# Performance work log

Measured on AMD Instinct MI355X. Metric: run time of the kernel, lower is better.

Reference implementation:

```python
import jax, jax.numpy as jnp
import numpy as np
from jax import lax

B, P, C = 2, 512, 5                 # images, proposals/img, classes (incl. background)
IN_FEAT, REP = 12544, 1024          # 256*7*7 pooled features; TwoMLPHead width
H_IMG = W_IMG = 800.0
SCORE_THRESH, NMS_THRESH, DET_PER_IMG = 0.05, 0.5, 100
MIN_SIZE = 0.01
WX, WY, WW, WH = 10.0, 10.0, 5.0, 5.0
BBOX_CLIP = float(np.log(1000.0 / 16.0))
NEG = -1e9


def _make_boxes(key, n):
    k1, k2, k3, k4 = jax.random.split(key, 4)
    cx = jax.random.uniform(k1, (n,)) * W_IMG
    cy = jax.random.uniform(k2, (n,)) * H_IMG
    bw = jax.random.uniform(k3, (n,)) * 180.0 + 20.0
    bh = jax.random.uniform(k4, (n,)) * 180.0 + 20.0
    x1 = jnp.clip(cx - bw / 2, 0.0, W_IMG)
    y1 = jnp.clip(cy - bh / 2, 0.0, H_IMG)
    x2 = jnp.clip(cx + bw / 2, 0.0, W_IMG)
    y2 = jnp.clip(cy + bh / 2, 0.0, H_IMG)
    return jnp.stack([x1, y1, x2, y2], -1).astype(jnp.float32)


def setup_inputs() -> dict:
    ks = jax.random.split(jax.random.key(0), 12)
    box_features = jax.random.normal(ks[0], (B * P, IN_FEAT), jnp.float32)
    proposals = jnp.stack([_make_boxes(ks[1 + i], P) for i in range(B)])
    def w(k, shp):
        return (jax.random.normal(k, shp, jnp.float32) / np.sqrt(shp[0])).astype(jnp.float32)
    return {
        'box_features': box_features,
        'proposals': proposals,
        'W1': w(ks[3], (IN_FEAT, REP)), 'b1': jnp.zeros((REP,), jnp.float32),
        'W2': w(ks[4], (REP, REP)),     'b2': jnp.zeros((REP,), jnp.float32),
        'Wc': w(ks[5], (REP, C)),       'bc': jnp.zeros((C,), jnp.float32),
        'Wb': w(ks[6], (REP, 4 * C)),   'bb': jnp.zeros((4 * C,), jnp.float32),
    }


def box_iou(a, b):
    area_a = (a[:, 2] - a[:, 0]) * (a[:, 3] - a[:, 1])
    area_b = (b[:, 2] - b[:, 0]) * (b[:, 3] - b[:, 1])
    lt = jnp.maximum(a[:, None, :2], b[None, :, :2])
    rb = jnp.minimum(a[:, None, 2:], b[None, :, 2:])
    wh = jnp.clip(rb - lt, 0.0)
    inter = wh[..., 0] * wh[..., 1]
    return inter / (area_a[:, None] + area_b[None, :] - inter + 1e-9)


def decode(reg, props):
    # reg: [N, C, 4] raw deltas; props: [N, 4] xyxy  (torchvision BoxCoder.decode)
    w = props[:, 2] - props[:, 0]
    h = props[:, 3] - props[:, 1]
    cx = props[:, 0] + 0.5 * w
    cy = props[:, 1] + 0.5 * h
    dx, dy = reg[..., 0] / WX, reg[..., 1] / WY
    dw = jnp.minimum(reg[..., 2] / WW, BBOX_CLIP)
    dh = jnp.minimum(reg[..., 3] / WH, BBOX_CLIP)
    pcx = dx * w[:, None] + cx[:, None]
    pcy = dy * h[:, None] + cy[:, None]
    pw = jnp.exp(dw) * w[:, None]
    ph = jnp.exp(dh) * h[:, None]
    return jnp.stack([pcx - 0.5 * pw, pcy - 0.5 * ph, pcx + 0.5 * pw, pcy + 0.5 * ph], -1)


def postprocess_one(boxes, scores, labels):
    # boxes [M,4] (already clipped), scores [M], labels [M] int; fixed-size output.
    M = boxes.shape[0]
    ws = boxes[:, 2] - boxes[:, 0]
    hs = boxes[:, 3] - boxes[:, 1]
    valid = (scores > SCORE_THRESH) & (ws >= MIN_SIZE) & (hs >= MIN_SIZE)
    order = jnp.argsort(-scores)
    b, s, l, v = boxes[order], scores[order], labels[order], valid[order]
    # batched (per-class) NMS via class-offset trick
    off = l.astype(b.dtype)[:, None] * (max(H_IMG, W_IMG) + 1.0)
    iou = box_iou(b + off, b + off)
    idxs = jnp.arange(M)

    def body(i, keep):
        sup = (iou[i] > NMS_THRESH) & keep[i] & (idxs > i)
        return keep & ~sup

    keep = lax.fori_loop(0, M, body, v)
    sc = jnp.where(keep, s, NEG)
    top_s, top_i = lax.top_k(sc, DET_PER_IMG)
    ok = top_s > NEG / 2
    tb = jnp.where(ok[:, None], b[top_i], 0.0)
    tl = jnp.where(ok, l[top_i], 0)
    ts = jnp.where(ok, top_s, 0.0)
    return tb, ts, tl


def reference(box_features, proposals, W1, b1, W2, b2, Wc, bc, Wb, bb):
    # box_head: TwoMLPHead
    h = jax.nn.relu(box_features @ W1 + b1)
    h = jax.nn.relu(h @ W2 + b2)
    # box_predictor
    class_logits = h @ Wc + bc                       # [N, C]
    box_regression = (h @ Wb + bb).reshape(-1, C, 4)  # [N, C, 4]
    props = proposals.reshape(-1, 4)
    pred = decode(box_regression, props)             # [N, C, 4]
    # clip to image
    pred = jnp.stack([
        jnp.clip(pred[..., 0], 0.0, W_IMG), jnp.clip(pred[..., 1], 0.0, H_IMG),
        jnp.clip(pred[..., 2], 0.0, W_IMG), jnp.clip(pred[..., 3], 0.0, H_IMG)], -1)
    scores = jax.nn.softmax(class_logits, -1)        # [N, C]
    # drop background class, flatten proposal-major (matches torch reshape(-1,4))
    pb = pred[:, 1:, :].reshape(B, P * (C - 1), 4)
    sc = scores[:, 1:].reshape(B, P * (C - 1))
    labels = jnp.tile(jnp.arange(1, C, dtype=jnp.int32), P)  # [M]
    boxes_o, scores_o, labels_o = jax.vmap(postprocess_one, in_axes=(0, 0, None))(pb, sc, labels)
    return boxes_o, scores_o, labels_o
```

## Files before the change

kernel.cpp:

```cpp
#include <hip/hip_runtime.h>
#include <math.h>

#define NROWS 1024
#define K1    12544
#define REP   1024
#define NDET  2048
#define DETS  100
#define BBOX_CLIP_F 4.135166556742356f
#define LDA   40

typedef __attribute__((ext_vector_type(8))) short bf16x8;
typedef __attribute__((ext_vector_type(4))) float f32x4;

__device__ __forceinline__ unsigned short rne_bf16(float x) {
  unsigned u = __float_as_uint(x);
  u += 0x7fffu + ((u >> 16) & 1u);
  return (unsigned short)(u >> 16);
}
__device__ __forceinline__ float bf16f(unsigned short h) {
  return __uint_as_float(((unsigned)h) << 16);
}

__global__ __launch_bounds__(256) void transpose_bf16(
    const float* __restrict__ W, unsigned short* __restrict__ WTh,
    unsigned short* __restrict__ WTl, int K, int N) {
  __shared__ unsigned short th[32 * 36], tl[32 * 36];
  const int k0 = blockIdx.x * 32, n0 = blockIdx.y * 32;
  const int t = threadIdx.x;
  const int r = t >> 3, c4 = (t & 7) << 2;
  float4 v = *(const float4*)&W[(size_t)(k0 + r) * N + n0 + c4];
  float fv[4] = {v.x, v.y, v.z, v.w};
#pragma unroll
  for (int j = 0; j < 4; ++j) {
    unsigned short h = rne_bf16(fv[j]);
    th[(c4 + j) * 36 + r] = h;
    tl[(c4 + j) * 36 + r] = rne_bf16(fv[j] - bf16f(h));
  }
  __syncthreads();
  ushort4 oh = *(ushort4*)&th[r * 36 + c4];
  ushort4 ol = *(ushort4*)&tl[r * 36 + c4];
  *(ushort4*)&WTh[(size_t)(n0 + r) * K + k0 + c4] = oh;
  *(ushort4*)&WTl[(size_t)(n0 + r) * K + k0 + c4] = ol;
}

__global__ __launch_bounds__(256) void gemm_mfma(
    const float* __restrict__ A, const unsigned short* __restrict__ BTh,
    const unsigned short* __restrict__ BTl, float* __restrict__ T,
    int K, int stepsPerZ) {
  __shared__ unsigned short Ash[128 * LDA], Asl[128 * LDA];
  __shared__ unsigned short Bsh[128 * LDA], Bsl[128 * LDA];
  const int tid = threadIdx.x;
  const int bm = blockIdx.x * 128, bn = blockIdx.y * 128;
  const int k0 = blockIdx.z * stepsPerZ * 32;
  const int w = tid >> 6, l = tid & 63;
  const int wr = (w >> 1) * 64, wc = (w & 1) * 64;
  const int fr = l & 15, fk = (l >> 4) * 8;
  const int srow = tid >> 2, skq = tid & 3;
  f32x4 acc[4][4];
#pragma unroll
  for (int m = 0; m < 4; ++m)
#pragma unroll
    for (int n = 0; n < 4; ++n) acc[m][n] = (f32x4){0.f, 0.f, 0.f, 0.f};

  for (int s = 0; s < stepsPerZ; ++s) {
    const int kk = k0 + s * 32;
#pragma unroll
    for (int half = 0; half < 2; ++half) {
      const int row = srow + half * 64;
      const float* ap = A + (size_t)(bm + row) * K + kk + skq * 8;
      float4 f0 = *(const float4*)ap;
      float4 f1 = *(const float4*)(ap + 4);
      float fv[8] = {f0.x, f0.y, f0.z, f0.w, f1.x, f1.y, f1.z, f1.w};
      unsigned hp[4], lp[4];
#pragma unroll
      for (int j = 0; j < 4; ++j) {
        unsigned short h0 = rne_bf16(fv[2 * j]), h1 = rne_bf16(fv[2 * j + 1]);
        float l0 = fv[2 * j] - bf16f(h0), l1 = fv[2 * j + 1] - bf16f(h1);
        hp[j] = (unsigned)h0 | ((unsigned)h1 << 16);
        lp[j] = (unsigned)rne_bf16(l0) | ((unsigned)rne_bf16(l1) << 16);
      }
      *(uint4*)&Ash[row * LDA + skq * 8] = make_uint4(hp[0], hp[1], hp[2], hp[3]);
      *(uint4*)&Asl[row * LDA + skq * 8] = make_uint4(lp[0], lp[1], lp[2], lp[3]);
      *(uint4*)&Bsh[row * LDA + skq * 8] =
          *(const uint4*)&BTh[(size_t)(bn + row) * K + kk + skq * 8];
      *(uint4*)&Bsl[row * LDA + skq * 8] =
          *(const uint4*)&BTl[(size_t)(bn + row) * K + kk + skq * 8];
    }
    __syncthreads();
    bf16x8 ah[4], al[4], bh[4], bl[4];
#pragma unroll
    for (int m = 0; m < 4; ++m) {
      ah[m] = *(const bf16x8*)&Ash[(wr + m * 16 + fr) * LDA + fk];
      al[m] = *(const bf16x8*)&Asl[(wr + m * 16 + fr) * LDA + fk];
    }
#pragma unroll
    for (int n = 0; n < 4; ++n) {
      bh[n] = *(const bf16x8*)&Bsh[(wc + n * 16 + fr) * LDA + fk];
      bl[n] = *(const bf16x8*)&Bsl[(wc + n * 16 + fr) * LDA + fk];
    }
#pragma unroll
    for (int m = 0; m < 4; ++m)
#pragma unroll
      for (int n = 0; n < 4; ++n) {
        acc[m][n] = __builtin_amdgcn_mfma_f32_16x16x32_bf16(ah[m], bh[n], acc[m][n], 0, 0, 0);
        acc[m][n] = __builtin_amdgcn_mfma_f32_16x16x32_bf16(ah[m], bl[n], acc[m][n], 0, 0, 0);
        acc[m][n] = __builtin_amdgcn_mfma_f32_16x16x32_bf16(al[m], bh[n], acc[m][n], 0, 0, 0);
      }
    __syncthreads();
  }
  float* Tz = T + (size_t)blockIdx.z * (NROWS * REP);
#pragma unroll
  for (int m = 0; m < 4; ++m) {
    const int r0 = bm + wr + m * 16 + ((l >> 4) << 2);
#pragma unroll
    for (int n = 0; n < 4; ++n) {
      const int c = bn + wc + n * 16 + fr;
#pragma unroll
      for (int j = 0; j < 4; ++j) Tz[(size_t)(r0 + j) * REP + c] = acc[m][n][j];
    }
  }
}

__global__ __launch_bounds__(256) void combine8_relu(
    const float* __restrict__ T, const float* __restrict__ bias, float* __restrict__ H) {
  const int i = blockIdx.x * 256 + threadIdx.x;
  const int MN4 = NROWS * REP / 4;
  const float4* t = (const float4*)T;
  float4 s0 = t[i];
#pragma unroll
  for (int z = 1; z < 8; ++z) {
    float4 v = t[i + z * MN4];
    s0.x += v.x; s0.y += v.y; s0.z += v.z; s0.w += v.w;
  }
  float4 bs = ((const float4*)bias)[i & 255];
  float4 r;
  r.x = fmaxf(s0.x + bs.x, 0.f);
  r.y = fmaxf(s0.y + bs.y, 0.f);
  r.z = fmaxf(s0.z + bs.z, 0.f);
  r.w = fmaxf(s0.w + bs.w, 0.f);
  ((float4*)H)[i] = r;
}

__global__ __launch_bounds__(256) void gemm64(
    const float* __restrict__ A, const float* __restrict__ W,
    float* __restrict__ T, int K, int N, int kChunk) {
  __shared__ float As[32][68];
  __shared__ float Bs[32][64];
  const int tid = threadIdx.x;
  const int bm = blockIdx.x * 64, bn = blockIdx.y * 64;
  const int k0 = blockIdx.z * kChunk;
  const int tx = tid & 15, ty = tid >> 4;
  const int ar = tid >> 3;
  const int ac = (tid & 7) << 2;
  const int br = tid >> 4;
  const int bc = (tid & 15) << 2;
  float acc[4][4] = {{0.f,0.f,0.f,0.f},{0.f,0.f,0.f,0.f},{0.f,0.f,0.f,0.f},{0.f,0.f,0.f,0.f}};
  for (int kk = k0; kk < k0 + kChunk; kk += 32) {
    float4 a0 = *(const float4*)&A[(size_t)(bm + ar) * K + kk + ac];
    float4 a1 = *(const float4*)&A[(size_t)(bm + ar + 32) * K + kk + ac];
    float4 b0 = *(const float4*)&W[(size_t)(kk + br) * N + bn + bc];
    float4 b1 = *(const float4*)&W[(size_t)(kk + br + 16) * N + bn + bc];
    As[ac+0][ar] = a0.x; As[ac+1][ar] = a0.y; As[ac+2][ar] = a0.z; As[ac+3][ar] = a0.w;
    As[ac+0][ar+32] = a1.x; As[ac+1][ar+32] = a1.y; As[ac+2][ar+32] = a1.z; As[ac+3][ar+32] = a1.w;
    *(float4*)&Bs[br][bc]    = b0;
    *(float4*)&Bs[br+16][bc] = b1;
    __syncthreads();
#pragma unroll
    for (int k = 0; k < 32; ++k) {
      float4 av = *(const float4*)&As[k][ty << 2];
      float4 bv = *(const float4*)&Bs[k][tx << 2];
      float a_[4] = {av.x, av.y, av.z, av.w};
      float b_[4] = {bv.x, bv.y, bv.z, bv.w};
#pragma unroll
      for (int i = 0; i < 4; ++i)
#pragma unroll
        for (int j = 0; j < 4; ++j)
          acc[i][j] = fmaf(a_[i], b_[j], acc[i][j]);
    }
    __syncthreads();
  }
  float* Tz = T + (size_t)blockIdx.z * NROWS * REP;
#pragma unroll
  for (int i = 0; i < 4; ++i) {
    float4 v = make_float4(acc[i][0], acc[i][1], acc[i][2], acc[i][3]);
    *(float4*)&Tz[(size_t)(bm + (ty << 2) + i) * N + bn + (tx << 2)] = v;
  }
}

__global__ __launch_bounds__(256) void combine_relu(
    const float* __restrict__ T, const float* __restrict__ bias, float* __restrict__ H) {
  const int i = blockIdx.x * 256 + threadIdx.x;
  const int MN4 = NROWS * REP / 4;
  const float4* t = (const float4*)T;
  float4 a = t[i], b = t[i + MN4], c = t[i + 2 * MN4], d = t[i + 3 * MN4];
  float4 bs = ((const float4*)bias)[i & 255];
  float4 r;
  r.x = fmaxf(((a.x + b.x) + (c.x + d.x)) + bs.x, 0.f);
  r.y = fmaxf(((a.y + b.y) + (c.y + d.y)) + bs.y, 0.f);
  r.z = fmaxf(((a.z + b.z) + (c.z + d.z)) + bs.z, 0.f);
  r.w = fmaxf(((a.w + b.w) + (c.w + d.w)) + bs.w, 0.f);
  ((float4*)H)[i] = r;
}

__global__ __launch_bounds__(256) void heads_kernel(
    const float* __restrict__ H2, const float* __restrict__ Wc, const float* __restrict__ bcv,
    const float* __restrict__ Wb, const float* __restrict__ bbv,
    const float* __restrict__ props, float* __restrict__ pb, float* __restrict__ sc) {
  const int n = blockIdx.x;
  __shared__ float hrow[REP];
  __shared__ float part[25][8];
  __shared__ float outv[25];
  __shared__ float smax[5];
  const int tid = threadIdx.x;
  ((float4*)hrow)[tid] = ((const float4*)(H2 + (size_t)n * REP))[tid];
  __syncthreads();
  if (tid < 200) {
    const int o = tid >> 3, s = tid & 7;
    float a = 0.f;
    if (o < 5) {
      const float* w = Wc + o;
      for (int k = s * 128; k < s * 128 + 128; ++k) a = fmaf(hrow[k], w[(size_t)k * 5], a);
    } else {
      const float* w = Wb + (o - 5);
      for (int k = s * 128; k < s * 128 + 128; ++k) a = fmaf(hrow[k], w[(size_t)k * 20], a);
    }
    part[o][s] = a;
  }
  __syncthreads();
  if (tid < 25) {
    float a = ((part[tid][0] + part[tid][1]) + (part[tid][2] + part[tid][3]))
            + ((part[tid][4] + part[tid][5]) + (part[tid][6] + part[tid][7]));
    a += (tid < 5) ? bcv[tid] : bbv[tid - 5];
    outv[tid] = a;
  }
  __syncthreads();
  if (tid == 0) {
    float m = outv[0];
    for (int c = 1; c < 5; ++c) m = fmaxf(m, outv[c]);
    float e[5], ssum = 0.f;
    for (int c = 0; c < 5; ++c) { e[c] = expf(outv[c] - m); ssum += e[c]; }
    for (int c = 0; c < 5; ++c) smax[c] = e[c] / ssum;
  }
  __syncthreads();
  if (tid < 4) {
    const int c = tid + 1;
    const float* pr = props + (size_t)n * 4;
    const float x1 = pr[0], y1 = pr[1], x2 = pr[2], y2 = pr[3];
    const float w = x2 - x1, h = y2 - y1;
    const float cx = x1 + 0.5f * w, cy = y1 + 0.5f * h;
    const float r0 = outv[5 + c * 4 + 0], r1 = outv[5 + c * 4 + 1];
    const float r2 = outv[5 + c * 4 + 2], r3 = outv[5 + c * 4 + 3];
    const float dx = r0 / 10.0f, dy = r1 / 10.0f;
    const float dw = fminf(r2 / 5.0f, BBOX_CLIP_F);
    const float dh = fminf(r3 / 5.0f, BBOX_CLIP_F);
    const float pcx = dx * w + cx, pcy = dy * h + cy;
    const float pw = expf(dw) * w, ph = expf(dh) * h;
    float bx1 = pcx - 0.5f * pw, by1 = pcy - 0.5f * ph;
    float bx2 = pcx + 0.5f * pw, by2 = pcy + 0.5f * ph;
    bx1 = fminf(fmaxf(bx1, 0.f), 800.f);
    by1 = fminf(fmaxf(by1, 0.f), 800.f);
    bx2 = fminf(fmaxf(bx2, 0.f), 800.f);
    by2 = fminf(fmaxf(by2, 0.f), 800.f);
    const int img = n >> 9;
    const int pidx = ((n & 511) << 2) + (c - 1);
    float* o = pb + (size_t)(img * NDET + pidx) * 4;
    o[0] = bx1; o[1] = by1; o[2] = bx2; o[3] = by2;
    sc[img * NDET + pidx] = smax[c];
  }
}

__global__ __launch_bounds__(1024) void sort_kernel(
    const float* __restrict__ sc, unsigned* __restrict__ sidx) {
  const int b = blockIdx.x;
  __shared__ unsigned long long key[NDET];
  const int tid = threadIdx.x;
  for (int t = tid; t < NDET; t += 1024) {
    unsigned bits = __float_as_uint(sc[b * NDET + t]);
    key[t] = ((unsigned long long)bits << 32) | (unsigned)(~t);
  }
  __syncthreads();
  for (int k = 2; k <= NDET; k <<= 1) {
    for (int j = k >> 1; j > 0; j >>= 1) {
      for (int t = tid; t < NDET; t += 1024) {
        const int ixj = t ^ j;
        if (ixj > t) {
          const bool up = (t & k) == 0;
          unsigned long long a = key[t], bb_ = key[ixj];
          if ((a < bb_) == up) { key[t] = bb_; key[ixj] = a; }
        }
      }
      __syncthreads();
    }
  }
  for (int t = tid; t < NDET; t += 1024)
    sidx[b * NDET + t] = ~(unsigned)key[t];
}

__global__ __launch_bounds__(256) void prep_kernel(
    const unsigned* __restrict__ sidx, const float* __restrict__ pb, const float* __restrict__ sc,
    float* __restrict__ sbox, float* __restrict__ soff, float* __restrict__ sscore,
    float* __restrict__ sarea, float* __restrict__ slab, unsigned* __restrict__ vword) {
  const int b = blockIdx.y;
  const int i = blockIdx.x * 256 + threadIdx.x;
  const unsigned oi = sidx[b * NDET + i];
  const float* bx = pb + (size_t)(b * NDET + oi) * 4;
  const float x1 = bx[0], y1 = bx[1], x2 = bx[2], y2 = bx[3];
  const float s = sc[b * NDET + oi];
  const float lab = (float)((oi & 3) + 1);
  const bool valid = (s > 0.05f) && ((x2 - x1) >= 0.01f) && ((y2 - y1) >= 0.01f);
  const float off = lab * 801.0f;
  float* sb = sbox + (size_t)(b * NDET + i) * 4;
  sb[0] = x1; sb[1] = y1; sb[2] = x2; sb[3] = y2;
  float* so = soff + (size_t)(b * NDET + i) * 4;
  so[0] = x1 + off; so[1] = y1 + off; so[2] = x2 + off; so[3] = y2 + off;
  sscore[b * NDET + i] = s;
  sarea[b * NDET + i] = (x2 - x1) * (y2 - y1);
  slab[b * NDET + i] = lab;
  const unsigned long long bal = __ballot(valid);
  if ((i & 31) == 0) vword[b * 64 + (i >> 5)] = (unsigned)(bal >> (i & 32));
}

__global__ __launch_bounds__(256) void mask_kernel(
    const float* __restrict__ soff, const float* __restrict__ sarea,
    unsigned* __restrict__ mask) {
  const int b = blockIdx.y;
  __shared__ float box[NDET][4];
  __shared__ float area[NDET];
  const int tid = threadIdx.x;
  const float4* src = (const float4*)(soff + (size_t)b * NDET * 4);
  for (int t = tid; t < NDET; t += 256) ((float4*)box)[t] = src[t];
  const float4* asrc = (const float4*)(sarea + (size_t)b * NDET);
  for (int t = tid; t < NDET / 4; t += 256) ((float4*)area)[t] = asrc[t];
  __syncthreads();
  const int li = tid >> 6;
  const int w  = tid & 63;
  const int i  = blockIdx.x * 4 + li;
  const float ax1 = box[i][0], ay1 = box[i][1], ax2 = box[i][2], ay2 = box[i][3];
  const float aa = area[i];
  unsigned bits = 0;
#pragma unroll 4
  for (int jj = 0; jj < 32; ++jj) {
    const int j = jj * 64 + w;
    const float ix = fmaxf(fminf(ax2, box[j][2]) - fmaxf(ax1, box[j][0]), 0.f);
    const float iy = fmaxf(fminf(ay2, box[j][3]) - fmaxf(ay1, box[j][1]), 0.f);
    const float inter = ix * iy;
    const float iou = inter / (aa + area[j] - inter + 1e-9f);
    if (j > i && iou > 0.5f) bits |= (1u << jj);
  }
  mask[((size_t)b * NDET + i) * 64 + w] = bits;
}

__global__ __launch_bounds__(64) void scan_kernel(
    const unsigned* __restrict__ vword, const unsigned* __restrict__ mask,
    const float* __restrict__ sbox, const float* __restrict__ sscore,
    const float* __restrict__ slab, float* __restrict__ out) {
  const int b = blockIdx.x;
  const int lane = threadIdx.x;
  const unsigned valid = vword[b * 64 + lane];
  unsigned sup = 0;
  __shared__ unsigned short klist[DETS];
  int kcnt = 0;
  for (int i = 0; i < NDET; ++i) {
    const unsigned v = __shfl(valid, i >> 5);
    if (!((v >> (i & 31)) & 1)) continue;
    const unsigned s = __shfl(sup, i & 63);
    if ((s >> (i >> 6)) & 1) continue;
    if (lane == 0) klist[kcnt] = (unsigned short)i;
    kcnt++;
    sup |= mask[((size_t)b * NDET + i) * 64 + lane];
    if (kcnt == DETS) break;
  }
  __syncthreads();
  for (int s = lane; s < DETS; s += 64) {
    float b0 = 0.f, b1 = 0.f, b2 = 0.f, b3 = 0.f, sv = 0.f, lv = 0.f;
    if (s < kcnt) {
      const int i = klist[s];
      const float* bx = sbox + ((size_t)b * NDET + i) * 4;
      b0 = bx[0]; b1 = bx[1]; b2 = bx[2]; b3 = bx[3];
      sv = sscore[b * NDET + i];
      lv = slab[b * NDET + i];
    }
    float* ob = out + ((size_t)b * DETS + s) * 4;
    ob[0] = b0; ob[1] = b1; ob[2] = b2; ob[3] = b3;
    out[2 * DETS * 4 + b * DETS + s] = sv;
    out[2 * DETS * 4 + 2 * DETS + b * DETS + s] = lv;
  }
}

extern "C" void kernel_launch(void* const* d_in, const int* in_sizes, int n_in,
                              void* d_out, int out_size, void* d_ws, size_t ws_size,
                              hipStream_t stream) {
  const float* X     = (const float*)d_in[0];
  const float* props = (const float*)d_in[1];
  const float* W1    = (const float*)d_in[2];
  const float* b1    = (const float*)d_in[3];
  const float* W2    = (const float*)d_in[4];
  const float* b2    = (const float*)d_in[5];
  const float* Wc    = (const float*)d_in[6];
  const float* bc    = (const float*)d_in[7];
  const float* Wb    = (const float*)d_in[8];
  const float* bb    = (const float*)d_in[9];
  float* out = (float*)d_out;

  const size_t NEED_MFMA =
      (size_t)(8 + 1 + 1) * 1048576 * 4 +
      (size_t)2 * (size_t)K1 * 1024 * 2 +
      (size_t)2 * 1048576 * 2 +
      (size_t)2500000;

  float *T, *H1, *H2, *pb, *sc;
  unsigned short *WTh = nullptr, *WTl = nullptr, *W2Th = nullptr, *W2Tl = nullptr;
  const bool use_mfma = (ws_size >= NEED_MFMA);
  if (use_mfma) {
    T   = (float*)d_ws;
    H1  = T + 8 * 1048576;
    H2  = H1 + 1048576;
    WTh = (unsigned short*)(H2 + 1048576);
    WTl = WTh + (size_t)K1 * 1024;
    W2Th = WTl + (size_t)K1 * 1024;
    W2Tl = W2Th + 1048576;
    pb  = (float*)(W2Tl + 1048576);
  } else {
    T  = (float*)d_ws;
    H1 = T + 4 * 1048576;
    H2 = H1 + 1048576;
    pb = H2 + 1048576;
  }
  sc = pb + 2 * NDET * 4;
  unsigned* sidx = (unsigned*)(sc + 2 * NDET);
  float* sbox   = (float*)(sidx + 2 * NDET);
  float* soff   = sbox + 2 * NDET * 4;
  float* sscore = soff + 2 * NDET * 4;
  float* sarea  = sscore + 2 * NDET;
  float* slab   = sarea + 2 * NDET;
  unsigned* vword = (unsigned*)(slab + 2 * NDET);
  unsigned* mask  = vword + 128;

  if (use_mfma) {
    transpose_bf16<<<dim3(K1 / 32, 32), 256, 0, stream>>>(W1, WTh, WTl, K1, REP);
    transpose_bf16<<<dim3(32, 32), 256, 0, stream>>>(W2, W2Th, W2Tl, REP, REP);
    gemm_mfma<<<dim3(8, 8, 8), 256, 0, stream>>>(X, WTh, WTl, T, K1, 49);
    combine8_relu<<<1024, 256, 0, stream>>>(T, b1, H1);
    gemm_mfma<<<dim3(8, 8, 4), 256, 0, stream>>>(H1, W2Th, W2Tl, T, REP, 8);
    combine_relu<<<1024, 256, 0, stream>>>(T, b2, H2);
  } else {
    gemm64<<<dim3(16, 16, 4), 256, 0, stream>>>(X, W1, T, K1, REP, K1 / 4);
    combine_relu<<<1024, 256, 0, stream>>>(T, b1, H1);
    gemm64<<<dim3(16, 16, 4), 256, 0, stream>>>(H1, W2, T, REP, REP, REP / 4);
    combine_relu<<<1024, 256, 0, stream>>>(T, b2, H2);
  }
  heads_kernel<<<1024, 256, 0, stream>>>(H2, Wc, bc, Wb, bb, props, pb, sc);
  sort_kernel<<<2, 1024, 0, stream>>>(sc, sidx);
  prep_kernel<<<dim3(8, 2), 256, 0, stream>>>(sidx, pb, sc, sbox, soff, sscore, sarea, slab, vword);
  mask_kernel<<<dim3(512, 2), 256, 0, stream>>>(soff, sarea, mask);
  scan_kernel<<<2, 64, 0, stream>>>(vword, mask, sbox, sscore, slab, out);
}
```

Baseline: 263.1 us.

## Pre-pack weights into swizzled tiles and double-buffer GEMM with direct LDS loads

The weight transpose kernel is replaced by a packer that writes bf16 hi/lo weights into tile-contiguous, XOR-swizzled 128x32 blocks. The GEMM then streams those blocks straight into LDS with global_load_lds and double-buffers both A and B, so the next k-step's loads overlap the current MFMAs and bank conflicts are avoided without padding. The second GEMM's split-K is raised from 4 to 8 so it matches combine8_relu. In exchange the kernel uses twice the LDS and more registers, which can lower occupancy.

Result: no change. 267.5 us (+1.7%).

```diff
diff --git a/kernel.cpp b/kernel.cpp
--- a/kernel.cpp
+++ b/kernel.cpp
@@ -7,7 +7,6 @@
 #define NDET  2048
 #define DETS  100
 #define BBOX_CLIP_F 4.135166556742356f
-#define LDA   40
 
 typedef __attribute__((ext_vector_type(8))) short bf16x8;
 typedef __attribute__((ext_vector_type(4))) float f32x4;
@@ -20,15 +19,23 @@
 __device__ __forceinline__ float bf16f(unsigned short h) {
   return __uint_as_float(((unsigned)h) << 16);
 }
-
-__global__ __launch_bounds__(256) void transpose_bf16(
-    const float* __restrict__ W, unsigned short* __restrict__ WTh,
-    unsigned short* __restrict__ WTl, int K, int N) {
+__device__ __forceinline__ int swz(int r, int s) {
+  return s ^ (r & 3) ^ ((r >> 2) & 3);
+}
+__device__ __forceinline__ void gload16(const void* g, void* lds) {
+  __builtin_amdgcn_global_load_lds(
+      (const __attribute__((address_space(1))) unsigned int*)g,
+      (__attribute__((address_space(3))) unsigned int*)lds, 16, 0, 0);
+}
+
+__global__ __launch_bounds__(256) void pack_b(
+    const float* __restrict__ W, unsigned short* __restrict__ Oh,
+    unsigned short* __restrict__ Ol, int nKB) {
   __shared__ unsigned short th[32 * 36], tl[32 * 36];
-  const int k0 = blockIdx.x * 32, n0 = blockIdx.y * 32;
+  const int kb = blockIdx.x, n0 = blockIdx.y * 32;
   const int t = threadIdx.x;
   const int r = t >> 3, c4 = (t & 7) << 2;
-  float4 v = *(const float4*)&W[(size_t)(k0 + r) * N + n0 + c4];
+  float4 v = *(const float4*)&W[(size_t)(kb * 32 + r) * REP + n0 + c4];
   float fv[4] = {v.x, v.y, v.z, v.w};
 #pragma unroll
   for (int j = 0; j < 4; ++j) {
@@ -37,66 +44,100 @@
     tl[(c4 + j) * 36 + r] = rne_bf16(fv[j] - bf16f(h));
   }
   __syncthreads();
-  ushort4 oh = *(ushort4*)&th[r * 36 + c4];
-  ushort4 ol = *(ushort4*)&tl[r * 36 + c4];
-  *(ushort4*)&WTh[(size_t)(n0 + r) * K + k0 + c4] = oh;
-  *(ushort4*)&WTl[(size_t)(n0 + r) * K + k0 + c4] = ol;
-}
-
-__global__ __launch_bounds__(256) void gemm_mfma(
-    const float* __restrict__ A, const unsigned short* __restrict__ BTh,
-    const unsigned short* __restrict__ BTl, float* __restrict__ T,
-    int K, int stepsPerZ) {
-  __shared__ unsigned short Ash[128 * LDA], Asl[128 * LDA];
-  __shared__ unsigned short Bsh[128 * LDA], Bsl[128 * LDA];
+  const int half = t >> 7;
+  const int n_loc = (t & 127) >> 2, slot = t & 3;
+  const unsigned short* src = (half ? tl : th) + n_loc * 36 + slot * 8;
+  ushort4 u0 = *(const ushort4*)src;
+  ushort4 u1 = *(const ushort4*)(src + 4);
+  const int n = n0 + n_loc, rb = n >> 7, rr = n & 127;
+  size_t chunk = ((size_t)(rb * nKB + kb)) * 512 + rr * 4 + swz(rr, slot);
+  unsigned short* dst = (half ? Ol : Oh) + chunk * 8;
+  *(ushort4*)dst = u0;
+  *(ushort4*)(dst + 4) = u1;
+}
+
+__global__ __launch_bounds__(256) void gemm_pk(
+    const float* __restrict__ A, const unsigned short* __restrict__ Bh,
+    const unsigned short* __restrict__ Bl, float* __restrict__ T,
+    int K, int nKB, int stepsPerZ) {
+  __shared__ __align__(16) unsigned short lds[2][4][4096];
   const int tid = threadIdx.x;
-  const int bm = blockIdx.x * 128, bn = blockIdx.y * 128;
-  const int k0 = blockIdx.z * stepsPerZ * 32;
   const int w = tid >> 6, l = tid & 63;
+  const int bm = blockIdx.x * 128;
+  const int bnb = blockIdx.y;
+  const int tk0 = blockIdx.z * stepsPerZ;
+  const int arow = tid >> 1, ahalf = tid & 1;
+  const int fr = l & 15, q = l >> 4;
   const int wr = (w >> 1) * 64, wc = (w & 1) * 64;
-  const int fr = l & 15, fk = (l >> 4) * 8;
-  const int srow = tid >> 2, skq = tid & 3;
+  const int qs = q ^ (fr & 3) ^ (fr >> 2);
+  const int aoff = ((wr + fr) * 4 + qs) * 16;
+  const int boff = ((wc + fr) * 4 + qs) * 16;
+  const float* aptr = A + (size_t)(bm + arow) * K + ahalf * 16;
+
+  float4 av[4];
+  auto loadA = [&](int tk) {
+    const float* p = aptr + tk * 32;
+#pragma unroll
+    for (int j = 0; j < 4; ++j) av[j] = *(const float4*)(p + j * 4);
+  };
+  auto stageB = [&](int bf, int tk) {
+    const unsigned short* gh = Bh + ((size_t)(bnb * nKB + tk)) * 4096;
+    const unsigned short* gl_ = Bl + ((size_t)(bnb * nKB + tk)) * 4096;
+#pragma unroll
+    for (int rseg = 0; rseg < 2; ++rseg) {
+      const int seg = rseg * 4 + w;
+      gload16(gh + (size_t)(seg * 64 + l) * 8, &lds[bf][2][seg * 512]);
+      gload16(gl_ + (size_t)(seg * 64 + l) * 8, &lds[bf][3][seg * 512]);
+    }
+  };
+  auto writeA = [&](int bf) {
+#pragma unroll
+    for (int j = 0; j < 2; ++j) {
+      const int s_ = ahalf * 2 + j;
+      float fv[8] = {av[j * 2].x, av[j * 2].y, av[j * 2].z, av[j * 2].w,
+                     av[j * 2 + 1].x, av[j * 2 + 1].y, av[j * 2 + 1].z, av[j * 2 + 1].w};
+      unsigned hp[4], lp[4];
+#pragma unroll
+      for (int p2 = 0; p2 < 4; ++p2) {
+        unsigned short h0 = rne_bf16(fv[2 * p2]), h1 = rne_bf16(fv[2 * p2 + 1]);
+        float l0 = fv[2 * p2] - bf16f(h0), l1 = fv[2 * p2 + 1] - bf16f(h1);
+        hp[p2] = (unsigned)h0 | ((unsigned)h1 << 16);
+        lp[p2] = (unsigned)rne_bf16(l0) | ((unsigned)rne_bf16(l1) << 16);
+      }
+      const int chunk = arow * 4 + swz(arow, s_);
+      *(uint4*)&lds[bf][0][chunk * 8] = make_uint4(hp[0], hp[1], hp[2], hp[3]);
+      *(uint4*)&lds[bf][1][chunk * 8] = make_uint4(lp[0], lp[1], lp[2], lp[3]);
+    }
+  };
+
   f32x4 acc[4][4];
 #pragma unroll
   for (int m = 0; m < 4; ++m)
 #pragma unroll
     for (int n = 0; n < 4; ++n) acc[m][n] = (f32x4){0.f, 0.f, 0.f, 0.f};
 
+  loadA(tk0);
+  stageB(0, tk0);
+  writeA(0);
+  __syncthreads();
+  int cur = 0;
   for (int s = 0; s < stepsPerZ; ++s) {
-    const int kk = k0 + s * 32;
-#pragma unroll
-    for (int half = 0; half < 2; ++half) {
-      const int row = srow + half * 64;
-      const float* ap = A + (size_t)(bm + row) * K + kk + skq * 8;
-      float4 f0 = *(const float4*)ap;
-      float4 f1 = *(const float4*)(ap + 4);
-      float fv[8] = {f0.x, f0.y, f0.z, f0.w, f1.x, f1.y, f1.z, f1.w};
-      unsigned hp[4], lp[4];
-#pragma unroll
-      for (int j = 0; j < 4; ++j) {
-        unsigned short h0 = rne_bf16(fv[2 * j]), h1 = rne_bf16(fv[2 * j + 1]);
-        float l0 = fv[2 * j] - bf16f(h0), l1 = fv[2 * j + 1] - bf16f(h1);
-        hp[j] = (unsigned)h0 | ((unsigned)h1 << 16);
-        lp[j] = (unsigned)rne_bf16(l0) | ((unsigned)rne_bf16(l1) << 16);
-      }
-      *(uint4*)&Ash[row * LDA + skq * 8] = make_uint4(hp[0], hp[1], hp[2], hp[3]);
-      *(uint4*)&Asl[row * LDA + skq * 8] = make_uint4(lp[0], lp[1], lp[2], lp[3]);
-      *(uint4*)&Bsh[row * LDA + skq * 8] =
-          *(const uint4*)&BTh[(size_t)(bn + row) * K + kk + skq * 8];
-      *(uint4*)&Bsl[row * LDA + skq * 8] =
-          *(const uint4*)&BTl[(size_t)(bn + row) * K + kk + skq * 8];
-    }
-    __syncthreads();
+    const bool nx = (s + 1 < stepsPerZ);
+    if (nx) { loadA(tk0 + s + 1); stageB(cur ^ 1, tk0 + s + 1); }
+    const char* La = (const char*)&lds[cur][0][0];
+    const char* Ll = (const char*)&lds[cur][1][0];
+    const char* Lbh = (const char*)&lds[cur][2][0];
+    const char* Lbl = (const char*)&lds[cur][3][0];
     bf16x8 ah[4], al[4], bh[4], bl[4];
 #pragma unroll
     for (int m = 0; m < 4; ++m) {
-      ah[m] = *(const bf16x8*)&Ash[(wr + m * 16 + fr) * LDA + fk];
-      al[m] = *(const bf16x8*)&Asl[(wr + m * 16 + fr) * LDA + fk];
+      ah[m] = *(const bf16x8*)(La + aoff + m * 1024);
+      al[m] = *(const bf16x8*)(Ll + aoff + m * 1024);
     }
 #pragma unroll
     for (int n = 0; n < 4; ++n) {
-      bh[n] = *(const bf16x8*)&Bsh[(wc + n * 16 + fr) * LDA + fk];
-      bl[n] = *(const bf16x8*)&Bsl[(wc + n * 16 + fr) * LDA + fk];
+      bh[n] = *(const bf16x8*)(Lbh + boff + n * 1024);
+      bl[n] = *(const bf16x8*)(Lbl + boff + n * 1024);
     }
 #pragma unroll
     for (int m = 0; m < 4; ++m)
@@ -106,7 +147,9 @@
         acc[m][n] = __builtin_amdgcn_mfma_f32_16x16x32_bf16(ah[m], bl[n], acc[m][n], 0, 0, 0);
         acc[m][n] = __builtin_amdgcn_mfma_f32_16x16x32_bf16(al[m], bh[n], acc[m][n], 0, 0, 0);
       }
+    if (nx) writeA(cur ^ 1);
     __syncthreads();
+    cur ^= 1;
   }
   float* Tz = T + (size_t)blockIdx.z * (NROWS * REP);
 #pragma unroll
@@ -114,7 +157,7 @@
     const int r0 = bm + wr + m * 16 + ((l >> 4) << 2);
 #pragma unroll
     for (int n = 0; n < 4; ++n) {
-      const int c = bn + wc + n * 16 + fr;
+      const int c = bnb * 128 + wc + n * 16 + fr;
 #pragma unroll
       for (int j = 0; j < 4; ++j) Tz[(size_t)(r0 + j) * REP + c] = acc[m][n][j];
     }
@@ -409,17 +452,17 @@
       (size_t)2500000;
 
   float *T, *H1, *H2, *pb, *sc;
-  unsigned short *WTh = nullptr, *WTl = nullptr, *W2Th = nullptr, *W2Tl = nullptr;
+  unsigned short *W1h = nullptr, *W1l = nullptr, *W2h = nullptr, *W2l = nullptr;
   const bool use_mfma = (ws_size >= NEED_MFMA);
   if (use_mfma) {
     T   = (float*)d_ws;
     H1  = T + 8 * 1048576;
     H2  = H1 + 1048576;
-    WTh = (unsigned short*)(H2 + 1048576);
-    WTl = WTh + (size_t)K1 * 1024;
-    W2Th = WTl + (size_t)K1 * 1024;
-    W2Tl = W2Th + 1048576;
-    pb  = (float*)(W2Tl + 1048576);
+    W1h = (unsigned short*)(H2 + 1048576);
+    W1l = W1h + (size_t)K1 * 1024;
+    W2h = W1l + (size_t)K1 * 1024;
+    W2l = W2h + 1048576;
+    pb  = (float*)(W2l + 1048576);
   } else {
     T  = (float*)d_ws;
     H1 = T + 4 * 1048576;
@@ -437,12 +480,12 @@
   unsigned* mask  = vword + 128;
 
   if (use_mfma) {
-    transpose_bf16<<<dim3(K1 / 32, 32), 256, 0, stream>>>(W1, WTh, WTl, K1, REP);
-    transpose_bf16<<<dim3(32, 32), 256, 0, stream>>>(W2, W2Th, W2Tl, REP, REP);
-    gemm_mfma<<<dim3(8, 8, 8), 256, 0, stream>>>(X, WTh, WTl, T, K1, 49);
+    pack_b<<<dim3(K1 / 32, 32), 256, 0, stream>>>(W1, W1h, W1l, K1 / 32);
+    pack_b<<<dim3(32, 32), 256, 0, stream>>>(W2, W2h, W2l, 32);
+    gemm_pk<<<dim3(8, 8, 8), 256, 0, stream>>>(X, W1h, W1l, T, K1, K1 / 32, 49);
     combine8_relu<<<1024, 256, 0, stream>>>(T, b1, H1);
-    gemm_mfma<<<dim3(8, 8, 4), 256, 0, stream>>>(H1, W2Th, W2Tl, T, REP, 8);
-    combine_relu<<<1024, 256, 0, stream>>>(T, b2, H2);
+    gemm_pk<<<dim3(8, 8, 8), 256, 0, stream>>>(H1, W2h, W2l, T, REP, 32, 4);
+    combine8_relu<<<1024, 256, 0, stream>>>(T, b2, H2);
   } else {
     gemm64<<<dim3(16, 16, 4), 256, 0, stream>>>(X, W1, T, K1, REP, K1 / 4);
     combine_relu<<<1024, 256, 0, stream>>>(T, b1, H1);
```
